# Performance work log

Measured on AMD Instinct MI355X. Metric: run time of the kernel, lower is better.

The kernel has to match this reference:

```python
import jax, jax.numpy as jnp
import numpy as np

N_HEADS, N_MODES, C_IN, C_OUT, SPD = 4, 32, 32, 32, 3


def setup_inputs() -> dict:
    key = jax.random.key(0)
    ks = jax.random.split(key, 9)
    B, NX, NY, NZ = 2, 48, 48, 48
    omega, c = 30.0 / 300.0, 6.0
    a = jax.random.normal(ks[0], (B, NX, NY, NZ, C_IN), jnp.float32)
    x = jax.random.uniform(ks[1], (B, NX, NY, NZ, SPD), jnp.float32)
    y = jax.random.uniform(ks[2], (B, NX, NY, NZ, SPD), jnp.float32)
    a_scale = np.sqrt(c / (C_IN + N_MODES)).astype(np.float32)
    x_scale = (np.sqrt(c / (SPD + N_MODES)) * omega).astype(np.float32)
    u_scale = np.sqrt(c / (N_HEADS * N_MODES + C_OUT)).astype(np.float32)
    a_modes = a_scale * (2 * jax.random.uniform(ks[3], (N_HEADS, N_MODES, C_IN), jnp.float32) - 1)
    x_modes = x_scale * (2 * jax.random.uniform(ks[4], (N_HEADS, N_MODES, SPD), jnp.float32) - 1)
    y_modes = x_scale * (2 * jax.random.uniform(ks[5], (N_HEADS, N_MODES, SPD), jnp.float32) - 1)
    u_modes = u_scale * (2 * jax.random.uniform(ks[6], (N_HEADS, N_MODES, C_OUT), jnp.float32) - 1)
    lim = 1.0 / np.sqrt(C_IN)
    fc_w = jax.random.uniform(ks[7], (C_OUT, C_IN), jnp.float32, -lim, lim)
    fc_b = jax.random.uniform(ks[8], (C_OUT,), jnp.float32, -lim, lim)
    return dict(a=a, x=x, y=y, a_modes=a_modes, x_modes=x_modes,
                y_modes=y_modes, u_modes=u_modes, fc_w=fc_w, fc_b=fc_b)


def _spectral_attention(a, x, y, a_modes, x_modes, y_modes, u_modes):
    # a: (b,nx,ny,nz,i); x,y: (b,nx,ny,nz,d)
    A = jnp.einsum('bxyzi,hfi->bhxyzf', a, a_modes)  # real
    X = jnp.exp(-2j * np.pi * jnp.einsum('bxyzd,hgd->bhxyzg', x, x_modes))
    Y = jnp.exp(2j * np.pi * jnp.einsum('bxyzd,hgd->bhxyzg', y, y_modes))
    n_xyz = y.shape[1] * y.shape[2] * y.shape[3]
    AX = jnp.einsum('bhxyzf,bhxyzg->bhfg', A.astype(X.dtype), X)
    U = jnp.einsum('bhfg,bhxyzg->bhxyzf', AX, Y).real / n_xyz
    return jnp.einsum('bhxyzf,hfo->bxyzo', U, u_modes)


def reference(a, x, y, a_modes, x_modes, y_modes, u_modes, fc_w, fc_b):
    att = _spectral_attention(a, x, y, a_modes, x_modes, y_modes, u_modes)
    skip = jnp.einsum('bxyzi,oi->bxyzo', a, fc_w) + fc_b
    return jax.nn.gelu(att + skip, approximate=False)
```

## Files before the change

### kernel.cpp

```cpp
#include <hip/hip_runtime.h>
#include <hip/hip_bf16.h>
#include <math.h>

#define NHEADS 4
#define NM 32
#define CIN 32
#define COUT 32
#define BATCH 2
#define NPTS (48*48*48)
#define PAD 36
#define SEGS_AX (NPTS/256)
#define SEGS_OUT (NPTS/128)
#define INV_N (1.0f / (float)NPTS)

typedef unsigned short ushort_t;
typedef __attribute__((ext_vector_type(8))) short short8;
typedef __attribute__((ext_vector_type(16))) float floatx16;

#define MFMA32 __builtin_amdgcn_mfma_f32_32x32x16_bf16

union frag8 { short8 v; uint2 u2[2]; unsigned u[4]; ushort_t s[8]; };

__device__ __forceinline__ floatx16 zero16() {
    floatx16 z;
#pragma unroll
    for (int i = 0; i < 16; ++i) z[i] = 0.0f;
    return z;
}
__device__ __forceinline__ ushort_t f2bf(float f) {
    __hip_bfloat16 h = __float2bfloat16(f);
    return *(ushort_t*)&h;
}
__device__ __forceinline__ float bf2f(ushort_t u) {
    union { unsigned i; float f; } v; v.i = ((unsigned)u) << 16; return v.f;
}
__device__ __forceinline__ unsigned pk2(float a, float b) {
    return (unsigned)f2bf(a) | ((unsigned)f2bf(b) << 16);
}
__device__ __forceinline__ short8 frag_from_f32(const float* __restrict__ p, float scale) {
    float4 f0 = ((const float4*)p)[0], f1 = ((const float4*)p)[1];
    frag8 r;
    r.u[0] = pk2(f0.x * scale, f0.y * scale);
    r.u[1] = pk2(f0.z * scale, f0.w * scale);
    r.u[2] = pk2(f1.x * scale, f1.y * scale);
    r.u[3] = pk2(f1.z * scale, f1.w * scale);
    return r.v;
}
__device__ __forceinline__ short8 frag_lds(const ushort_t* p) {
    frag8 r;
    r.u2[0] = *(const uint2*)p;
    r.u2[1] = *(const uint2*)(p + 4);
    return r.v;
}

__global__ __launch_bounds__(256, 3) void k_ax(
    const float* __restrict__ a, const float* __restrict__ x,
    const float* __restrict__ a_modes, const float* __restrict__ x_modes,
    float* __restrict__ AX, float* __restrict__ part, int use_part)
{
    __shared__ ushort_t s_a[256][PAD];
    __shared__ float    s_xT[3][256];
    __shared__ ushort_t s_At[NHEADS][NM][PAD];
    __shared__ ushort_t s_Xre[NHEADS][NM][PAD];
    __shared__ ushort_t s_Xim[NHEADS][NM][PAD];

    const int t = threadIdx.x;
    const int w = t >> 6;
    const int l = t & 63;
    const int l31 = l & 31, lh = l >> 5;
    const int b  = blockIdx.x / SEGS_AX;
    const int sb = blockIdx.x % SEGS_AX;
    const int pbase = b * NPTS + sb * 256;

    {
        const float* arow = a + (size_t)(pbase + t) * CIN;
        unsigned* dst = (unsigned*)&s_a[t][0];
#pragma unroll
        for (int v = 0; v < 8; ++v) {
            float4 f = ((const float4*)arow)[v];
            dst[2*v]   = pk2(f.x, f.y);
            dst[2*v+1] = pk2(f.z, f.w);
        }
        for (int idx = t; idx < 256*3; idx += 256)
            s_xT[idx % 3][idx / 3] = x[(size_t)pbase * 3 + idx];
    }
    short8 amf[2];
#pragma unroll
    for (int kh = 0; kh < 2; ++kh)
        amf[kh] = frag_from_f32(a_modes + (w*NM + l31)*CIN + kh*16 + lh*8, 1.0f);
    const float xm0 = x_modes[(w*NM + l31)*3 + 0];
    const float xm1 = x_modes[(w*NM + l31)*3 + 1];
    const float xm2 = x_modes[(w*NM + l31)*3 + 2];

    floatx16 accre = zero16(), accim = zero16();
    __syncthreads();

    for (int c = 0; c < 8; ++c) {
        const int p0 = c * 32;
        floatx16 dA = zero16();
#pragma unroll
        for (int kh = 0; kh < 2; ++kh) {
            short8 af = frag_lds(&s_a[p0 + l31][kh*16 + lh*8]);
            dA = MFMA32(amf[kh], af, dA, 0, 0, 0);
        }
#pragma unroll
        for (int r = 0; r < 16; ++r) {
            const int fr = (r & 3) + 8*(r >> 2) + 4*lh;
            s_At[w][fr][l31] = f2bf(dA[r]);
        }
#pragma unroll
        for (int j = 0; j < 16; j += 2) {
            const int pl = lh*16 + j;
            const int pt = p0 + pl;
            const float px0 = s_xT[0][pt]*xm0 + s_xT[1][pt]*xm1 + s_xT[2][pt]*xm2;
            const float px1 = s_xT[0][pt+1]*xm0 + s_xT[1][pt+1]*xm1 + s_xT[2][pt+1]*xm2;
            *(unsigned*)&s_Xre[w][l31][pl] =
                pk2(__builtin_amdgcn_cosf(px0), __builtin_amdgcn_cosf(px1));
            *(unsigned*)&s_Xim[w][l31][pl] =
                pk2(-__builtin_amdgcn_sinf(px0), -__builtin_amdgcn_sinf(px1));
        }
#pragma unroll
        for (int kh = 0; kh < 2; ++kh) {
            short8 atf = frag_lds(&s_At[w][l31][kh*16 + lh*8]);
            short8 xrf = frag_lds(&s_Xre[w][l31][kh*16 + lh*8]);
            short8 xif = frag_lds(&s_Xim[w][l31][kh*16 + lh*8]);
            accre = MFMA32(atf, xrf, accre, 0, 0, 0);
            accim = MFMA32(atf, xif, accim, 0, 0, 0);
        }
    }

    if (use_part) {
        float* pr = part + (size_t)blockIdx.x * 8192;
#pragma unroll
        for (int r = 0; r < 16; ++r) {
            const int fr = (r & 3) + 8*(r >> 2) + 4*lh;
            const int idx = (w*NM + fr)*NM + l31;
            pr[idx]        = accre[r];
            pr[idx + 4096] = accim[r];
        }
    } else {
        float* AXre = AX;
        float* AXim = AX + BATCH*NHEADS*NM*NM;
#pragma unroll
        for (int r = 0; r < 16; ++r) {
            const int fr = (r & 3) + 8*(r >> 2) + 4*lh;
            const int idx = b*4096 + (w*NM + fr)*NM + l31;
            atomicAdd(&AXre[idx], accre[r]);
            atomicAdd(&AXim[idx], accim[r]);
        }
    }
}

__global__ void k_red(const float* __restrict__ part, float* __restrict__ AX)
{
    __shared__ float s_red[4][64];
    const int t = threadIdx.x, q = t >> 6, l = t & 63;
    const int o = blockIdx.x * 64 + l;
    const int bb = o >> 13;
    const int idx = o & 8191;
    float acc = 0.f;
#pragma unroll 4
    for (int sb = q; sb < SEGS_AX; sb += 4)
        acc += part[((size_t)(bb*SEGS_AX + sb))*8192 + idx];
    s_red[q][l] = acc;
    __syncthreads();
    if (q == 0) {
        const float s = s_red[0][l] + s_red[1][l] + s_red[2][l] + s_red[3][l];
        if (idx < 4096) AX[bb*4096 + idx] = s;
        else            AX[8192 + bb*4096 + (idx - 4096)] = s;
    }
}

__global__ __launch_bounds__(256, 3) void k_out(
    const float* __restrict__ a, const float* __restrict__ y,
    const float* __restrict__ y_modes, const float* __restrict__ u_modes,
    const float* __restrict__ fc_w, const float* __restrict__ fc_b,
    const float* __restrict__ AX, float* __restrict__ out)
{
    __shared__ ushort_t s_umT[NHEADS][NM][PAD];
    __shared__ float    s_ym[NHEADS][NM][3];
    __shared__ float    s_yT[3][128];
    __shared__ ushort_t s_ah[128][PAD];
    __shared__ ushort_t s_Yre[4][NM][PAD];
    __shared__ ushort_t s_Yim[4][NM][PAD];
    __shared__ ushort_t s_U[4][NM][PAD];

    const int t = threadIdx.x, w = t >> 6, l = t & 63;
    const int l31 = l & 31, lh = l >> 5;
    const int b  = blockIdx.x / SEGS_OUT;
    const int sb = blockIdx.x % SEGS_OUT;
    const int pblock = b * NPTS + sb * 128;
    const int pwave  = pblock + w * 32;

    for (int idx = t; idx < NHEADS*NM*NM; idx += 256) {
        const int h = idx >> 10, f = (idx >> 5) & 31, o = idx & 31;
        s_umT[h][o][f] = f2bf(u_modes[idx]);
    }
    for (int idx = t; idx < NHEADS*NM*3; idx += 256)
        ((float*)s_ym)[idx] = y_modes[idx];
    for (int idx = t; idx < 128*3; idx += 256)
        s_yT[idx % 3][idx / 3] = y[(size_t)pblock * 3 + idx];
    if (t < 128) {
        const float* arow = a + (size_t)(pblock + t) * CIN;
        unsigned* dst = (unsigned*)&s_ah[t][0];
#pragma unroll
        for (int v = 0; v < 8; ++v) {
            float4 f = ((const float4*)arow)[v];
            dst[2*v]   = pk2(f.x, f.y);
            dst[2*v+1] = pk2(f.z, f.w);
        }
    }
    short8 axre[NHEADS][2], axim[NHEADS][2];
    {
        const float* AXre = AX;
        const float* AXim = AX + BATCH*NHEADS*NM*NM;
#pragma unroll
        for (int h = 0; h < NHEADS; ++h)
#pragma unroll
            for (int kh = 0; kh < 2; ++kh) {
                const int off = b*4096 + (h*NM + l31)*NM + kh*16 + lh*8;
                axre[h][kh] = frag_from_f32(AXre + off, INV_N);
                axim[h][kh] = frag_from_f32(AXim + off, INV_N);
            }
    }
    short8 whi[2], wlo[2];
#pragma unroll
    for (int kh = 0; kh < 2; ++kh) {
        const float* p = fc_w + l31*CIN + kh*16 + lh*8;
        float4 f0 = ((const float4*)p)[0], f1 = ((const float4*)p)[1];
        float v[8] = {f0.x,f0.y,f0.z,f0.w,f1.x,f1.y,f1.z,f1.w};
        frag8 hi, lo;
#pragma unroll
        for (int j = 0; j < 8; ++j) {
            const ushort_t hb = f2bf(v[j]);
            hi.s[j] = hb;
            lo.s[j] = f2bf(v[j] - bf2f(hb));
        }
        whi[kh] = hi.v; wlo[kh] = lo.v;
    }
    const float fb = fc_b[l31];

    __syncthreads();
    float y3[3];
#pragma unroll
    for (int d = 0; d < 3; ++d) y3[d] = s_yT[d][w*32 + l31];

    floatx16 acc = zero16();
#pragma unroll
    for (int kh = 0; kh < 2; ++kh) {
        short8 af = frag_lds(&s_ah[w*32 + l31][kh*16 + lh*8]);
        acc = MFMA32(af, whi[kh], acc, 0, 0, 0);
        acc = MFMA32(af, wlo[kh], acc, 0, 0, 0);
    }
    for (int h = 0; h < NHEADS; ++h) {
#pragma unroll
        for (int j = 0; j < 16; j += 2) {
            const int g0 = lh*16 + j;
            const float py0 = y3[0]*s_ym[h][g0][0]   + y3[1]*s_ym[h][g0][1]   + y3[2]*s_ym[h][g0][2];
            const float py1 = y3[0]*s_ym[h][g0+1][0] + y3[1]*s_ym[h][g0+1][1] + y3[2]*s_ym[h][g0+1][2];
            *(unsigned*)&s_Yre[w][l31][g0] =
                pk2(__builtin_amdgcn_cosf(py0), __builtin_amdgcn_cosf(py1));
            *(unsigned*)&s_Yim[w][l31][g0] =
                pk2(-__builtin_amdgcn_sinf(py0), -__builtin_amdgcn_sinf(py1));
        }
        floatx16 du = zero16();
#pragma unroll
        for (int kh = 0; kh < 2; ++kh) {
            short8 yr = frag_lds(&s_Yre[w][l31][kh*16 + lh*8]);
            short8 yi = frag_lds(&s_Yim[w][l31][kh*16 + lh*8]);
            du = MFMA32(yr, axre[h][kh], du, 0, 0, 0);
            du = MFMA32(yi, axim[h][kh], du, 0, 0, 0);
        }
#pragma unroll
        for (int r = 0; r < 16; ++r) {
            const int ptr_ = (r & 3) + 8*(r >> 2) + 4*lh;
            s_U[w][ptr_][l31] = f2bf(du[r]);
        }
#pragma unroll
        for (int kh = 0; kh < 2; ++kh) {
            short8 uf = frag_lds(&s_U[w][l31][kh*16 + lh*8]);
            short8 mf = frag_lds(&s_umT[h][l31][kh*16 + lh*8]);
            acc = MFMA32(uf, mf, acc, 0, 0, 0);
        }
    }
#pragma unroll
    for (int r = 0; r < 16; ++r) {
        const int ptr_ = (r & 3) + 8*(r >> 2) + 4*lh;
        const float z = acc[r] + fb;
        out[(size_t)(pwave + ptr_) * COUT + l31] =
            0.5f * z * (1.0f + erff(z * 0.70710678118654752f));
    }
}

extern "C" void kernel_launch(void* const* d_in, const int* in_sizes, int n_in,
                              void* d_out, int out_size, void* d_ws, size_t ws_size,
                              hipStream_t stream) {
    (void)in_sizes; (void)n_in; (void)out_size;
    const float* a       = (const float*)d_in[0];
    const float* x       = (const float*)d_in[1];
    const float* y       = (const float*)d_in[2];
    const float* a_modes = (const float*)d_in[3];
    const float* x_modes = (const float*)d_in[4];
    const float* y_modes = (const float*)d_in[5];
    const float* u_modes = (const float*)d_in[6];
    const float* fc_w    = (const float*)d_in[7];
    const float* fc_b    = (const float*)d_in[8];
    float* out  = (float*)d_out;
    float* AX   = (float*)d_ws;
    float* part = (float*)((char*)d_ws + 65536);

    const size_t need = 65536 + (size_t)BATCH * SEGS_AX * 8192 * sizeof(float);
    const int use_part = (ws_size >= need) ? 1 : 0;

    hipMemsetAsync(AX, 0, 65536, stream);
    k_ax<<<BATCH * SEGS_AX, 256, 0, stream>>>(a, x, a_modes, x_modes, AX, part, use_part);
    if (use_part) k_red<<<256, 256, 0, stream>>>(part, AX);
    k_out<<<BATCH * SEGS_OUT, 256, 0, stream>>>(a, y, y_modes, u_modes, fc_w, fc_b, AX, out);
}
```

Baseline: 169.6 us.

## Precompute AX·u_modes per head and build X/Y fragments directly in registers

Adds a small k_w kernel that multiplies the normalised AX matrices by u_modes once per batch and head, producing bf16 W matrices. k_out can then contract the Y phases straight against W, removing the per-point U intermediate, its LDS round trip and one MFMA stage per head. Both k_ax and k_out now compute cos/sin phase fragments in registers instead of staging them through LDS, which frees shared memory, and launch bounds rise from 3 to 4 blocks per CU. The reduction kernel is reshaped to use 8 partial rows per output column. The cost is one extra tiny launch and an extra bf16 rounding of the fused W product.

```diff
diff --git a/kernel.cpp b/kernel.cpp
--- a/kernel.cpp
+++ b/kernel.cpp
@@ -53,16 +53,14 @@
     return r.v;
 }
 
-__global__ __launch_bounds__(256, 3) void k_ax(
+__global__ __launch_bounds__(256, 4) void k_ax(
     const float* __restrict__ a, const float* __restrict__ x,
     const float* __restrict__ a_modes, const float* __restrict__ x_modes,
     float* __restrict__ AX, float* __restrict__ part, int use_part)
 {
     __shared__ ushort_t s_a[256][PAD];
-    __shared__ float    s_xT[3][256];
+    __shared__ float4   s_x4[256];
     __shared__ ushort_t s_At[NHEADS][NM][PAD];
-    __shared__ ushort_t s_Xre[NHEADS][NM][PAD];
-    __shared__ ushort_t s_Xim[NHEADS][NM][PAD];
 
     const int t = threadIdx.x;
     const int w = t >> 6;
@@ -81,8 +79,11 @@
             dst[2*v]   = pk2(f.x, f.y);
             dst[2*v+1] = pk2(f.z, f.w);
         }
-        for (int idx = t; idx < 256*3; idx += 256)
-            s_xT[idx % 3][idx / 3] = x[(size_t)pbase * 3 + idx];
+        for (int idx = t; idx < 256*3; idx += 256) {
+            const float v = x[(size_t)pbase * 3 + idx];
+            const int pt = idx / 3;
+            ((float*)&s_x4[pt])[idx - 3*pt] = v;
+        }
     }
     short8 amf[2];
 #pragma unroll
@@ -97,6 +98,21 @@
 
     for (int c = 0; c < 8; ++c) {
         const int p0 = c * 32;
+        short8 xre[2], xim[2];
+#pragma unroll
+        for (int kh = 0; kh < 2; ++kh) {
+            frag8 re_, im_;
+#pragma unroll
+            for (int j = 0; j < 8; j += 2) {
+                const int pl = p0 + kh*16 + lh*8 + j;
+                const float4 v0 = s_x4[pl], v1 = s_x4[pl + 1];
+                const float q0 = v0.x*xm0 + v0.y*xm1 + v0.z*xm2;
+                const float q1 = v1.x*xm0 + v1.y*xm1 + v1.z*xm2;
+                re_.u[j>>1] = pk2( __builtin_amdgcn_cosf(q0),  __builtin_amdgcn_cosf(q1));
+                im_.u[j>>1] = pk2(-__builtin_amdgcn_sinf(q0), -__builtin_amdgcn_sinf(q1));
+            }
+            xre[kh] = re_.v; xim[kh] = im_.v;
+        }
         floatx16 dA = zero16();
 #pragma unroll
         for (int kh = 0; kh < 2; ++kh) {
@@ -109,23 +125,10 @@
             s_At[w][fr][l31] = f2bf(dA[r]);
         }
 #pragma unroll
-        for (int j = 0; j < 16; j += 2) {
-            const int pl = lh*16 + j;
-            const int pt = p0 + pl;
-            const float px0 = s_xT[0][pt]*xm0 + s_xT[1][pt]*xm1 + s_xT[2][pt]*xm2;
-            const float px1 = s_xT[0][pt+1]*xm0 + s_xT[1][pt+1]*xm1 + s_xT[2][pt+1]*xm2;
-            *(unsigned*)&s_Xre[w][l31][pl] =
-                pk2(__builtin_amdgcn_cosf(px0), __builtin_amdgcn_cosf(px1));
-            *(unsigned*)&s_Xim[w][l31][pl] =
-                pk2(-__builtin_amdgcn_sinf(px0), -__builtin_amdgcn_sinf(px1));
-        }
-#pragma unroll
         for (int kh = 0; kh < 2; ++kh) {
             short8 atf = frag_lds(&s_At[w][l31][kh*16 + lh*8]);
-            short8 xrf = frag_lds(&s_Xre[w][l31][kh*16 + lh*8]);
-            short8 xif = frag_lds(&s_Xim[w][l31][kh*16 + lh*8]);
-            accre = MFMA32(atf, xrf, accre, 0, 0, 0);
-            accim = MFMA32(atf, xif, accim, 0, 0, 0);
+            accre = MFMA32(atf, xre[kh], accre, 0, 0, 0);
+            accim = MFMA32(atf, xim[kh], accim, 0, 0, 0);
         }
     }
 
@@ -153,37 +156,78 @@
 
 __global__ void k_red(const float* __restrict__ part, float* __restrict__ AX)
 {
-    __shared__ float s_red[4][64];
-    const int t = threadIdx.x, q = t >> 6, l = t & 63;
-    const int o = blockIdx.x * 64 + l;
-    const int bb = o >> 13;
-    const int idx = o & 8191;
+    __shared__ float s_red[8][32];
+    const int t = threadIdx.x, q = t >> 5, l = t & 31;
+    const int o = blockIdx.x * 32 + l;
+    const int bb = o >> 13, idx = o & 8191;
     float acc = 0.f;
-#pragma unroll 4
-    for (int sb = q; sb < SEGS_AX; sb += 4)
+#pragma unroll 6
+    for (int sb = q; sb < SEGS_AX; sb += 8)
         acc += part[((size_t)(bb*SEGS_AX + sb))*8192 + idx];
     s_red[q][l] = acc;
     __syncthreads();
-    if (q == 0) {
-        const float s = s_red[0][l] + s_red[1][l] + s_red[2][l] + s_red[3][l];
-        if (idx < 4096) AX[bb*4096 + idx] = s;
-        else            AX[8192 + bb*4096 + (idx - 4096)] = s;
-    }
-}
-
-__global__ __launch_bounds__(256, 3) void k_out(
+    if (t < 32) {
+        float s = 0.f;
+#pragma unroll
+        for (int qq = 0; qq < 8; ++qq) s += s_red[qq][t];
+        const int oo = blockIdx.x * 32 + t;
+        const int b2 = oo >> 13, i2 = oo & 8191;
+        if (i2 < 4096) AX[b2*4096 + i2] = s;
+        else           AX[8192 + b2*4096 + (i2 - 4096)] = s;
+    }
+}
+
+__global__ void k_w(const float* __restrict__ AX, const float* __restrict__ u_modes,
+                    ushort_t* __restrict__ W)
+{
+    const int t = threadIdx.x, w = t >> 6, l = t & 63;
+    const int l31 = l & 31, lh = l >> 5;
+    const int pair = blockIdx.x * 4 + w;
+    const int b = pair >> 2, h = pair & 3;
+    const float* AXre = AX + b*4096 + h*1024;
+    const float* AXim = AX + BATCH*4096 + b*4096 + h*1024;
+    const float* um   = u_modes + h*1024;
+
+    short8 umf[2], axr[2], axi[2];
+#pragma unroll
+    for (int kh = 0; kh < 2; ++kh) {
+        frag8 u_, r_, i_;
+#pragma unroll
+        for (int j = 0; j < 8; j += 2) {
+            const int f0 = kh*16 + lh*8 + j, f1 = f0 + 1;
+            u_.u[j>>1] = pk2(um[f0*32 + l31], um[f1*32 + l31]);
+            r_.u[j>>1] = pk2(AXre[f0*32 + l31]*INV_N, AXre[f1*32 + l31]*INV_N);
+            i_.u[j>>1] = pk2(AXim[f0*32 + l31]*INV_N, AXim[f1*32 + l31]*INV_N);
+        }
+        umf[kh] = u_.v; axr[kh] = r_.v; axi[kh] = i_.v;
+    }
+    floatx16 wre = zero16(), wim = zero16();
+#pragma unroll
+    for (int kh = 0; kh < 2; ++kh) {
+        wre = MFMA32(umf[kh], axr[kh], wre, 0, 0, 0);
+        wim = MFMA32(umf[kh], axi[kh], wim, 0, 0, 0);
+    }
+    ushort_t* Wre = W + (size_t)pair * 1024;
+    ushort_t* Wim = Wre + 8192;
+#pragma unroll
+    for (int r = 0; r < 16; ++r) {
+        const int o = (r & 3) + 8*(r >> 2) + 4*lh;
+        Wre[o*32 + l31] = f2bf(wre[r]);
+        Wim[o*32 + l31] = f2bf(wim[r]);
+    }
+}
+
+__global__ __launch_bounds__(256, 4) void k_out(
     const float* __restrict__ a, const float* __restrict__ y,
-    const float* __restrict__ y_modes, const float* __restrict__ u_modes,
+    const float* __restrict__ y_modes, const ushort_t* __restrict__ Wg,
     const float* __restrict__ fc_w, const float* __restrict__ fc_b,
-    const float* __restrict__ AX, float* __restrict__ out)
+    float* __restrict__ out)
 {
-    __shared__ ushort_t s_umT[NHEADS][NM][PAD];
-    __shared__ float    s_ym[NHEADS][NM][3];
-    __shared__ float    s_yT[3][128];
+    __shared__ ushort_t s_Wre[NHEADS][NM][PAD];
+    __shared__ ushort_t s_Wim[NHEADS][NM][PAD];
+    __shared__ float4   s_ym4[NHEADS][NM];
+    __shared__ float4   s_y4[128];
     __shared__ ushort_t s_ah[128][PAD];
-    __shared__ ushort_t s_Yre[4][NM][PAD];
-    __shared__ ushort_t s_Yim[4][NM][PAD];
-    __shared__ ushort_t s_U[4][NM][PAD];
 
     const int t = threadIdx.x, w = t >> 6, l = t & 63;
     const int l31 = l & 31, lh = l >> 5;
@@ -192,14 +236,26 @@
     const int pblock = b * NPTS + sb * 128;
     const int pwave  = pblock + w * 32;
 
-    for (int idx = t; idx < NHEADS*NM*NM; idx += 256) {
-        const int h = idx >> 10, f = (idx >> 5) & 31, o = idx & 31;
-        s_umT[h][o][f] = f2bf(u_modes[idx]);
-    }
-    for (int idx = t; idx < NHEADS*NM*3; idx += 256)
-        ((float*)s_ym)[idx] = y_modes[idx];
-    for (int idx = t; idx < 128*3; idx += 256)
-        s_yT[idx % 3][idx / 3] = y[(size_t)pblock * 3 + idx];
+    {
+        const unsigned* wr = (const unsigned*)Wg + b*2048;
+        const unsigned* wi = (const unsigned*)(Wg + 8192) + b*2048;
+        for (int idx2 = t; idx2 < 2048; idx2 += 256) {
+            const int h = idx2 >> 9, o = (idx2 >> 4) & 31, g2 = (idx2 & 15) * 2;
+            *(unsigned*)&s_Wre[h][o][g2] = wr[idx2];
+            *(unsigned*)&s_Wim[h][o][g2] = wi[idx2];
+        }
+    }
+    if (t < 128) {
+        const int h = t >> 5, g = t & 31;
+        const float* p = y_modes + (h*NM + g)*3;
+        float4 v; v.x = p[0]; v.y = p[1]; v.z = p[2]; v.w = 0.f;
+        s_ym4[h][g] = v;
+    }
+    for (int idx = t; idx < 128*3; idx += 256) {
+        const float v = y[(size_t)pblock * 3 + idx];
+        const int pt = idx / 3;
+        ((float*)&s_y4[pt])[idx - 3*pt] = v;
+    }
     if (t < 128) {
         const float* arow = a + (size_t)(pblock + t) * CIN;
         unsigned* dst = (unsigned*)&s_ah[t][0];
@@ -209,19 +265,6 @@
             dst[2*v]   = pk2(f.x, f.y);
             dst[2*v+1] = pk2(f.z, f.w);
         }
-    }
-    short8 axre[NHEADS][2], axim[NHEADS][2];
-    {
-        const float* AXre = AX;
-        const float* AXim = AX + BATCH*NHEADS*NM*NM;
-#pragma unroll
-        for (int h = 0; h < NHEADS; ++h)
-#pragma unroll
-            for (int kh = 0; kh < 2; ++kh) {
-                const int off = b*4096 + (h*NM + l31)*NM + kh*16 + lh*8;
-                axre[h][kh] = frag_from_f32(AXre + off, INV_N);
-                axim[h][kh] = frag_from_f32(AXim + off, INV_N);
-            }
     }
     short8 whi[2], wlo[2];
 #pragma unroll
@@ -241,9 +284,7 @@
     const float fb = fc_b[l31];
 
     __syncthreads();
-    float y3[3];
-#pragma unroll
-    for (int d = 0; d < 3; ++d) y3[d] = s_yT[d][w*32 + l31];
+    const float4 y3 = s_y4[w*32 + l31];
 
     floatx16 acc = zero16();
 #pragma unroll
@@ -253,34 +294,27 @@
         acc = MFMA32(af, wlo[kh], acc, 0, 0, 0);
     }
     for (int h = 0; h < NHEADS; ++h) {
-#pragma unroll
-        for (int j = 0; j < 16; j += 2) {
-            const int g0 = lh*16 + j;
-            const float py0 = y3[0]*s_ym[h][g0][0]   + y3[1]*s_ym[h][g0][1]   + y3[2]*s_ym[h][g0][2];
-            const float py1 = y3[0]*s_ym[h][g0+1][0] + y3[1]*s_ym[h][g0+1][1] + y3[2]*s_ym[h][g0+1][2];
-            *(unsigned*)&s_Yre[w][l31][g0] =
-                pk2(__builtin_amdgcn_cosf(py0), __builtin_amdgcn_cosf(py1));
-            *(unsigned*)&s_Yim[w][l31][g0] =
-                pk2(-__builtin_amdgcn_sinf(py0), -__builtin_amdgcn_sinf(py1));
-        }
-        floatx16 du = zero16();
-#pragma unroll
-        for (int kh = 0; kh < 2; ++kh) {
-            short8 yr = frag_lds(&s_Yre[w][l31][kh*16 + lh*8]);
-            short8 yi = frag_lds(&s_Yim[w][l31][kh*16 + lh*8]);
-            du = MFMA32(yr, axre[h][kh], du, 0, 0, 0);
-            du = MFMA32(yi, axim[h][kh], du, 0, 0, 0);
-        }
-#pragma unroll
-        for (int r = 0; r < 16; ++r) {
-            const int ptr_ = (r & 3) + 8*(r >> 2) + 4*lh;
-            s_U[w][ptr_][l31] = f2bf(du[r]);
-        }
-#pragma unroll
-        for (int kh = 0; kh < 2; ++kh) {
-            short8 uf = frag_lds(&s_U[w][l31][kh*16 + lh*8]);
-            short8 mf = frag_lds(&s_umT[h][l31][kh*16 + lh*8]);
-            acc = MFMA32(uf, mf, acc, 0, 0, 0);
+        short8 yre[2], yim[2];
+#pragma unroll
+        for (int kh = 0; kh < 2; ++kh) {
+            frag8 re_, im_;
+#pragma unroll
+            for (int j = 0; j < 8; j += 2) {
+                const int g0 = kh*16 + lh*8 + j;
+                const float4 m0 = s_ym4[h][g0], m1 = s_ym4[h][g0 + 1];
+                const float p0 = y3.x*m0.x + y3.y*m0.y + y3.z*m0.z;
+                const float p1 = y3.x*m1.x + y3.y*m1.y + y3.z*m1.z;
+                re_.u[j>>1] = pk2( __builtin_amdgcn_cosf(p0),  __builtin_amdgcn_cosf(p1));
+                im_.u[j>>1] = pk2(-__builtin_amdgcn_sinf(p0), -__builtin_amdgcn_sinf(p1));
+            }
+            yre[kh] = re_.v; yim[kh] = im_.v;
+        }
+#pragma unroll
+        for (int kh = 0; kh < 2; ++kh) {
+            short8 wrf = frag_lds(&s_Wre[h][l31][kh*16 + lh*8]);
+            short8 wif = frag_lds(&s_Wim[h][l31][kh*16 + lh*8]);
+            acc = MFMA32(yre[kh], wrf, acc, 0, 0, 0);
+            acc = MFMA32(yim[kh], wif, acc, 0, 0, 0);
         }
     }
 #pragma unroll
@@ -306,14 +340,16 @@
     const float* fc_w    = (const float*)d_in[7];
     const float* fc_b    = (const float*)d_in[8];
     float* out  = (float*)d_out;
-    float* AX   = (float*)d_ws;
-    float* part = (float*)((char*)d_ws + 65536);
-
-    const size_t need = 65536 + (size_t)BATCH * SEGS_AX * 8192 * sizeof(float);
+    float*    AX   = (float*)d_ws;
+    ushort_t* W    = (ushort_t*)((char*)d_ws + 65536);
+    float*    part = (float*)((char*)d_ws + 98304);
+
+    const size_t need = 98304 + (size_t)BATCH * SEGS_AX * 8192 * sizeof(float);
     const int use_part = (ws_size >= need) ? 1 : 0;
 
     hipMemsetAsync(AX, 0, 65536, stream);
     k_ax<<<BATCH * SEGS_AX, 256, 0, stream>>>(a, x, a_modes, x_modes, AX, part, use_part);
-    if (use_part) k_red<<<256, 256, 0, stream>>>(part, AX);
-    k_out<<<BATCH * SEGS_OUT, 256, 0, stream>>>(a, y, y_modes, u_modes, fc_w, fc_b, AX, out);
-}
+    if (use_part) k_red<<<512, 256, 0, stream>>>(part, AX);
+    k_w<<<2, 256, 0, stream>>>(AX, u_modes, W);
+    k_out<<<BATCH * SEGS_OUT, 256, 0, stream>>>(a, y, y_modes, W, fc_w, fc_b, out);
+}
```

After: 152.2 us. -10.3%, faster.
